# Kernel optimization log

Hardware: AMD Instinct MI355X
Metric: run time of the kernel (lower is better)

Reference implementation:

```python
import jax, jax.numpy as jnp
import numpy as np

N, D_IN, H, C, K = 16384, 2048, 4096, 256, 256


def setup_inputs() -> dict:
    key = jax.random.key(0)
    ks = jax.random.split(key, 13)

    def lin(kw, kb, fan_in, fan_out):
        # torch Linear default init: U(-1/sqrt(fan_in), 1/sqrt(fan_in)); stored as [in, out]
        bound = 1.0 / np.sqrt(fan_in)
        W = jax.random.uniform(kw, (fan_in, fan_out), jnp.float32, -bound, bound)
        b = jax.random.uniform(kb, (fan_out,), jnp.float32, -bound, bound)
        return W, b

    W_e1, b_e1 = lin(ks[0], ks[1], D_IN, H)
    W_e2, b_e2 = lin(ks[2], ks[3], H, C)
    W_d1, b_d1 = lin(ks[4], ks[5], C, H)
    W_d2, b_d2 = lin(ks[6], ks[7], H, D_IN)
    # codebooks init U(-1/K, 1/K) per the torch code
    cb1 = jax.random.uniform(ks[8], (K, C), jnp.float32, -1.0 / K, 1.0 / K)
    cb2 = jax.random.uniform(ks[9], (K, C), jnp.float32, -1.0 / K, 1.0 / K)
    cb3 = jax.random.uniform(ks[10], (K, C), jnp.float32, -1.0 / K, 1.0 / K)
    x = jax.random.normal(ks[11], (N, D_IN), jnp.float32)
    return {"x": x, "W_e1": W_e1, "b_e1": b_e1, "W_e2": W_e2, "b_e2": b_e2,
            "cb1": cb1, "cb2": cb2, "cb3": cb3,
            "W_d1": W_d1, "b_d1": b_d1, "W_d2": W_d2, "b_d2": b_d2}


def _vq_stage(z, cb):
    # dist[n,k] = sum_c (cb[k,c] - z[n,c])^2 = ||z||^2 - 2 z.cb^T + ||cb||^2
    # (same math as the torch N x K x C broadcast, expressed as a GEMM)
    d = (jnp.sum(z * z, axis=1, keepdims=True)
         - 2.0 * (z @ cb.T)
         + jnp.sum(cb * cb, axis=1))            # [N, K]
    nearest = jnp.argmin(d, axis=1)             # [N]
    zq = cb[nearest]                            # gather [N, C]
    return nearest, zq


def reference(x, W_e1, b_e1, W_e2, b_e2, cb1, cb2, cb3, W_d1, b_d1, W_d2, b_d2):
    ze_1 = jax.nn.relu(x @ W_e1 + b_e1) @ W_e2 + b_e2     # [N, C]
    nearest_1, zq_1 = _vq_stage(ze_1, cb1)
    ze_2 = ze_1 - zq_1
    nearest_2, zq_2 = _vq_stage(ze_2, cb2)
    ze_3 = ze_2 - zq_2
    nearest_3, zq_3 = _vq_stage(ze_3, cb3)
    # straight-through estimator
    decoder_input = ze_1 + jax.lax.stop_gradient(zq_1 + zq_2 + zq_3 - ze_1)
    x_hat = jax.nn.sigmoid(decoder_input @ W_d1 + b_d1) @ W_d2 + b_d2
    return (x_hat, ze_1, ze_2, ze_3, zq_1, zq_2, zq_3, nearest_1, nearest_2, nearest_3)
```

## Files before the change

kernel.cpp:

```cpp
#include <hip/hip_runtime.h>
#include <cstddef>


#define NN 16384
#define DIN 2048
#define HH 4096
#define CC 256
#define QRED ((size_t)4096 * 256)
#define NZ 24

typedef unsigned short ushortT;
typedef __attribute__((ext_vector_type(8))) short bf16x8;
typedef __attribute__((ext_vector_type(4))) float f32x4;

__device__ __forceinline__ ushortT f2b(float v) {
    unsigned int u = __float_as_uint(v);
    return (ushortT)((u + 0x7fffu + ((u >> 16) & 1u)) >> 16);
}
__device__ __forceinline__ float b2f(ushortT s) {
    return __uint_as_float(((unsigned int)s) << 16);
}
__device__ __forceinline__ void split3(float v, ushortT& h, ushortT& m, ushortT& l) {
    h = f2b(v);
    float r1 = v - b2f(h);
    m = f2b(r1);
    l = f2b(r1 - b2f(m));
}

__device__ __forceinline__ void gld16(const void* g, void* l) {
    __builtin_amdgcn_global_load_lds(
        (const __attribute__((address_space(1))) unsigned int*)g,
        (__attribute__((address_space(3))) unsigned int*)l,
        16, 0, 0);
}

template<int NP>
__launch_bounds__(256)
__global__ void tsplit(const float* __restrict__ W,
                       ushortT* __restrict__ T0,
                       ushortT* __restrict__ T1,
                       ushortT* __restrict__ T2,
                       int K, int N)
{
    __shared__ float tile[32][33];
    const int k0 = blockIdx.y * 32, n0 = blockIdx.x * 32;
    const int c = threadIdx.x & 31, r = threadIdx.x >> 5;
    #pragma unroll
    for (int i = 0; i < 4; ++i)
        tile[r + 8*i][c] = W[(size_t)(k0 + r + 8*i) * N + n0 + c];
    __syncthreads();
    #pragma unroll
    for (int i = 0; i < 4; ++i) {
        const int nl = r + 8*i, kl = c;
        float v = tile[kl][nl];
        size_t o = (size_t)(n0 + nl) * K + k0 + kl;
        ushortT h = f2b(v);
        T0[o] = h;
        if (NP > 1) {
            float r1 = v - b2f(h);
            ushortT m = f2b(r1);
            T1[o] = m;
            T2[o] = f2b(r1 - b2f(m));
        }
    }
}

__launch_bounds__(256)
__global__ void split_src(const float* __restrict__ X,
                          ushortT* __restrict__ P0, ushortT* __restrict__ P1,
                          ushortT* __restrict__ P2, size_t n4)
{
    for (size_t i = (size_t)blockIdx.x * 256 + threadIdx.x; i < n4;
         i += (size_t)gridDim.x * 256) {
        float4 v = *(const float4*)(X + i * 4);
        ushort4 hv, mv, lv;
        split3(v.x, ((ushortT*)&hv)[0], ((ushortT*)&mv)[0], ((ushortT*)&lv)[0]);
        split3(v.y, ((ushortT*)&hv)[1], ((ushortT*)&mv)[1], ((ushortT*)&lv)[1]);
        split3(v.z, ((ushortT*)&hv)[2], ((ushortT*)&mv)[2], ((ushortT*)&lv)[2]);
        split3(v.w, ((ushortT*)&hv)[3], ((ushortT*)&mv)[3], ((ushortT*)&lv)[3]);
        *(ushort4*)(P0 + i * 4) = hv;
        *(ushort4*)(P1 + i * 4) = mv;
        *(ushort4*)(P2 + i * 4) = lv;
    }
}

template<int NSEG, int KSH, int NTC, int EPI, int OM>
__launch_bounds__(512, 2)
__global__ void gemm256(const ushortT* __restrict__ Ab, size_t aPl,
                        const ushortT* __restrict__ Bb, size_t bPl,
                        const float* __restrict__ bias,
                        float* __restrict__ Cf,
                        ushortT* __restrict__ Ob, size_t oPl,
                        int N, int K)
{
    __shared__ ushortT sh[65536];

    const int t    = threadIdx.x;
    const int lane = t & 63;
    const int wid  = t >> 6;
    const int l15  = lane & 15;
    const int l4   = lane >> 4;
    const int bm   = blockIdx.y * 256;
    const int bn   = blockIdx.x * 256;
    const int wm   = (wid >> 2) * 128;
    const int wn   = (wid & 3) * 64;
    const int t0   = (OM == 3) ? blockIdx.z * NTC : 0;

    constexpr unsigned PA_PACK = 0x210100u;
    constexpr unsigned PB_PACK = 0x012010u;

    const int trow = t >> 3;
    const unsigned tcol = (unsigned)(((t & 7) ^ (trow & 7)) * 8);
    unsigned gA[4], gB[4];
    #pragma unroll
    for (int i = 0; i < 4; ++i) {
        gA[i] = (unsigned)(bm + i * 64 + trow) * (unsigned)K + tcol;
        gB[i] = (unsigned)(bn + i * 64 + trow) * (unsigned)K + tcol;
    }
    const int ldsT = t * 8;

    auto stageH = [&](int buf, int gtt, int half) {
        const int seg = (NSEG > 1) ? (gtt >> KSH) : 0;
        const unsigned kin = ((unsigned)(gtt & ((1 << KSH) - 1))) << 6;
        const unsigned pa = (NSEG > 1) ? ((PA_PACK >> (seg * 4)) & 15u) : 0u;
        const unsigned pb = (NSEG > 1) ? ((PB_PACK >> (seg * 4)) & 15u) : 0u;
        const ushortT* Abase = Ab + (size_t)pa * aPl + kin;
        const ushortT* Bbase = Bb + (size_t)pb * bPl + kin;
        ushortT* lb = sh + buf * 32768;
        if (half == 0) {
            gld16(Abase + gA[0], lb + 0 * 4096 + ldsT);
            gld16(Abase + gA[2], lb + 2 * 4096 + ldsT);
            gld16(Bbase + gB[0], lb + 16384 + 0 * 4096 + ldsT);
            gld16(Bbase + gB[1], lb + 16384 + 1 * 4096 + ldsT);
        } else {
            gld16(Bbase + gB[2], lb + 16384 + 2 * 4096 + ldsT);
            gld16(Bbase + gB[3], lb + 16384 + 3 * 4096 + ldsT);
            gld16(Abase + gA[1], lb + 1 * 4096 + ldsT);
            gld16(Abase + gA[3], lb + 3 * 4096 + ldsT);
        }
    };

    f32x4 acc[8][4] = {};

    stageH(0, t0, 0);
    stageH(0, t0, 1);

    #pragma unroll 1
    for (int tt = 0; tt < NTC; ++tt) {
        const int buf = tt & 1;
        const ushortT* As = sh + buf * 32768;
        const ushortT* Bs = As + 16384;
        const bool notlast = (tt + 1 < NTC);
        bf16x8 b0[4], a0[4], a1[4], b1[4], a2[4], a3[4];

        asm volatile("s_waitcnt vmcnt(0)" ::: "memory");
        __builtin_amdgcn_sched_barrier(0);
        __builtin_amdgcn_s_barrier();
        __builtin_amdgcn_sched_barrier(0);

        #pragma unroll
        for (int ni = 0; ni < 4; ++ni) {
            const int rb = wn + ni * 16 + l15;
            b0[ni] = *(const bf16x8*)&Bs[rb * 64 + (l4 ^ (rb & 7)) * 8];
        }
        #pragma unroll
        for (int mi = 0; mi < 4; ++mi) {
            const int ra = wm + mi * 16 + l15;
            a0[mi] = *(const bf16x8*)&As[ra * 64 + (l4 ^ (ra & 7)) * 8];
        }
        if (notlast) stageH(buf ^ 1, t0 + tt + 1, 0);
        __builtin_amdgcn_sched_barrier(0);
        __builtin_amdgcn_s_barrier();
        asm volatile("s_waitcnt lgkmcnt(0)" ::: "memory");
        __builtin_amdgcn_sched_barrier(0);
        __builtin_amdgcn_s_setprio(1);
        #pragma unroll
        for (int mi = 0; mi < 4; ++mi)
            #pragma unroll
            for (int ni = 0; ni < 4; ++ni)
                acc[mi][ni] = __builtin_amdgcn_mfma_f32_16x16x32_bf16(
                    a0[mi], b0[ni], acc[mi][ni], 0, 0, 0);
        __builtin_amdgcn_s_setprio(0);
        __builtin_amdgcn_sched_barrier(0);

        #pragma unroll
        for (int mi = 0; mi < 4; ++mi) {
            const int ra = wm + (mi + 4) * 16 + l15;
            a1[mi] = *(const bf16x8*)&As[ra * 64 + (l4 ^ (ra & 7)) * 8];
        }
        if (notlast) stageH(buf ^ 1, t0 + tt + 1, 1);
        __builtin_amdgcn_sched_barrier(0);
        __builtin_amdgcn_s_barrier();
        asm volatile("s_waitcnt lgkmcnt(0)" ::: "memory");
        __builtin_amdgcn_sched_barrier(0);
        __builtin_amdgcn_s_setprio(1);
        #pragma unroll
        for (int mi = 0; mi < 4; ++mi)
            #pragma unroll
            for (int ni = 0; ni < 4; ++ni)
                acc[mi + 4][ni] = __builtin_amdgcn_mfma_f32_16x16x32_bf16(
                    a1[mi], b0[ni], acc[mi + 4][ni], 0, 0, 0);
        __builtin_amdgcn_s_setprio(0);
        __builtin_amdgcn_sched_barrier(0);

        #pragma unroll
        for (int ni = 0; ni < 4; ++ni) {
            const int rb = wn + ni * 16 + l15;
            b1[ni] = *(const bf16x8*)&Bs[rb * 64 + ((4 | l4) ^ (rb & 7)) * 8];
        }
        #pragma unroll
        for (int mi = 0; mi < 4; ++mi) {
            const int ra = wm + mi * 16 + l15;
            a2[mi] = *(const bf16x8*)&As[ra * 64 + ((4 | l4) ^ (ra & 7)) * 8];
        }
        __builtin_amdgcn_sched_barrier(0);
        __builtin_amdgcn_s_barrier();
        asm volatile("s_waitcnt lgkmcnt(0)" ::: "memory");
        __builtin_amdgcn_sched_barrier(0);
        __builtin_amdgcn_s_setprio(1);
        #pragma unroll
        for (int mi = 0; mi < 4; ++mi)
            #pragma unroll
            for (int ni = 0; ni < 4; ++ni)
                acc[mi][ni] = __builtin_amdgcn_mfma_f32_16x16x32_bf16(
                    a2[mi], b1[ni], acc[mi][ni], 0, 0, 0);
        __builtin_amdgcn_s_setprio(0);
        __builtin_amdgcn_sched_barrier(0);

        #pragma unroll
        for (int mi = 0; mi < 4; ++mi) {
            const int ra = wm + (mi + 4) * 16 + l15;
            a3[mi] = *(const bf16x8*)&As[ra * 64 + ((4 | l4) ^ (ra & 7)) * 8];
        }
        __builtin_amdgcn_sched_barrier(0);
        __builtin_amdgcn_s_barrier();
        asm volatile("s_waitcnt lgkmcnt(0)" ::: "memory");
        __builtin_amdgcn_sched_barrier(0);
        __builtin_amdgcn_s_setprio(1);
        #pragma unroll
        for (int mi = 0; mi < 4; ++mi)
            #pragma unroll
            for (int ni = 0; ni < 4; ++ni)
                acc[mi + 4][ni] = __builtin_amdgcn_mfma_f32_16x16x32_bf16(
                    a3[mi], b1[ni], acc[mi + 4][ni], 0, 0, 0);
        __builtin_amdgcn_s_setprio(0);
        __builtin_amdgcn_sched_barrier(0);
    }

    #pragma unroll
    for (int ni = 0; ni < 4; ++ni) {
        const int gcol = bn + wn + ni * 16 + l15;
        float bvv = 0.0f;
        if (OM != 3) bvv = bias[gcol];
        #pragma unroll
        for (int mi = 0; mi < 8; ++mi) {
            #pragma unroll
            for (int r = 0; r < 4; ++r) {
                const int grow = bm + wm + mi * 16 + l4 * 4 + r;
                const size_t o = (size_t)grow * N + gcol;
                if (OM == 3) {
                    Cf[(size_t)blockIdx.z * oPl + o] = acc[mi][ni][r];
                } else {
                    float v = acc[mi][ni][r] + bvv;
                    if (EPI == 1) v = fmaxf(v, 0.0f);
                    if (EPI == 2) v = 1.0f / (1.0f + expf(-v));
                    if (OM == 0) {
                        Cf[o] = v;
                    } else if (OM == 2) {
                        Ob[o] = f2b(v);
                    } else {
                        ushortT hh, mm, ll;
                        split3(v, hh, mm, ll);
                        Ob[o] = hh; Ob[oPl + o] = mm; Ob[2 * oPl + o] = ll;
                    }
                }
            }
        }
    }
}

__launch_bounds__(256)
__global__ void reduce_z(const float* __restrict__ part,
                         const float* __restrict__ bias,
                         float* __restrict__ outp, int n4)
{
    const int i = blockIdx.x * 256 + threadIdx.x;
    if (i >= n4) return;
    float4 s = *(const float4*)(part + (size_t)i * 4);
    #pragma unroll
    for (int z = 1; z < NZ; ++z) {
        float4 p = *(const float4*)(part + (size_t)z * (QRED) + (size_t)i * 4);
        s.x = __fadd_rn(s.x, p.x); s.y = __fadd_rn(s.y, p.y);
        s.z = __fadd_rn(s.z, p.z); s.w = __fadd_rn(s.w, p.w);
    }
    const int c4 = (i * 4) & 255;
    float4 b = *(const float4*)(bias + c4);
    s.x = __fadd_rn(s.x, b.x); s.y = __fadd_rn(s.y, b.y);
    s.z = __fadd_rn(s.z, b.z); s.w = __fadd_rn(s.w, b.w);
    *(float4*)(outp + (size_t)i * 4) = s;
}

__launch_bounds__(256)
__global__ void vq_kernel(const float* __restrict__ ze1,
                          const float* __restrict__ cb1,
                          const float* __restrict__ cb2,
                          const float* __restrict__ cb3,
                          float* __restrict__ out_ze2, float* __restrict__ out_ze3,
                          float* __restrict__ out_zq1, float* __restrict__ out_zq2,
                          float* __restrict__ out_zq3,
                          float* __restrict__ out_n1,  float* __restrict__ out_n2,
                          float* __restrict__ out_n3,
                          ushortT* __restrict__ dec_p)
{
    __shared__ float Zs[16][260];
    __shared__ float Ds[16][260];
    __shared__ float DecS[16][260];
    __shared__ float Srow[16];
    __shared__ int   Kmin[16];

    const int t    = threadIdx.x;
    const int row0 = blockIdx.x * 16;

    for (int i = t; i < 16*64; i += 256) {
        int r = i >> 6, c4 = (i & 63) << 2;
        float4 v = *(const float4*)(ze1 + (size_t)(row0 + r) * 256 + c4);
        *(float4*)&Zs[r][c4] = v;
        float4 z = {0.f,0.f,0.f,0.f};
        *(float4*)&DecS[r][c4] = z;
    }
    __syncthreads();

    const float* cbs[3] = {cb1, cb2, cb3};
    float* zqs[3] = {out_zq1, out_zq2, out_zq3};
    float* nss[3] = {out_n1, out_n2, out_n3};

    for (int s = 0; s < 3; ++s) {
        const float* cb = cbs[s];
        if (t < 16) {
            float ssum = 0.f;
            for (int c = 0; c < 256; ++c) ssum = fmaf(Zs[t][c], Zs[t][c], ssum);
            Srow[t] = ssum;
        }
        __syncthreads();
        {
            float accr[16];
            #pragma unroll
            for (int r = 0; r < 16; ++r) accr[r] = 0.f;
            float c2 = 0.f;
            const float* cbrow = cb + (size_t)t * 256;
            for (int c4 = 0; c4 < 256; c4 += 4) {
                float4 cv = *(const float4*)(cbrow + c4);
                c2 = fmaf(cv.x,cv.x,fmaf(cv.y,cv.y,fmaf(cv.z,cv.z,fmaf(cv.w,cv.w,c2))));
                #pragma unroll
                for (int r = 0; r < 16; ++r) {
                    float4 zv = *(const float4*)&Zs[r][c4];
                    accr[r] = fmaf(zv.x,cv.x,fmaf(zv.y,cv.y,
                              fmaf(zv.z,cv.z,fmaf(zv.w,cv.w,accr[r]))));
                }
            }
            #pragma unroll
            for (int r = 0; r < 16; ++r) {
                float g2 = __fmul_rn(2.0f, accr[r]);
                float t1 = __fsub_rn(Srow[r], g2);
                Ds[r][t]  = __fadd_rn(t1, c2);
            }
        }
        __syncthreads();
        if (t < 16) {
            float best = Ds[t][0];
            int bk = 0;
            for (int k = 1; k < 256; ++k) {
                float v = Ds[t][k];
                if (v < best) { best = v; bk = k; }
            }
            Kmin[t] = bk;
            nss[s][row0 + t] = (float)bk;
        }
        __syncthreads();
        for (int i = t; i < 16*64; i += 256) {
            int r = i >> 6, c4 = (i & 63) << 2;
            const float* q = cb + (size_t)Kmin[r] * 256 + c4;
            float4 qv = *(const float4*)q;
            *(float4*)&zqs[s][(size_t)(row0 + r) * 256 + c4] = qv;
            float4 dv = *(float4*)&DecS[r][c4];
            dv.x = __fadd_rn(dv.x, qv.x); dv.y = __fadd_rn(dv.y, qv.y);
            dv.z = __fadd_rn(dv.z, qv.z); dv.w = __fadd_rn(dv.w, qv.w);
            *(float4*)&DecS[r][c4] = dv;
            if (s < 2) {
                float4 zv = *(float4*)&Zs[r][c4];
                zv.x = __fsub_rn(zv.x, qv.x); zv.y = __fsub_rn(zv.y, qv.y);
                zv.z = __fsub_rn(zv.z, qv.z); zv.w = __fsub_rn(zv.w, qv.w);
                *(float4*)&Zs[r][c4] = zv;
                float* oz = (s == 0) ? out_ze2 : out_ze3;
                *(float4*)&oz[(size_t)(row0 + r) * 256 + c4] = zv;
            }
        }
        __syncthreads();
    }

    for (int i = t; i < 16*64; i += 256) {
        int r = i >> 6, c4 = (i & 63) << 2;
        float4 z1 = *(const float4*)(ze1 + (size_t)(row0 + r) * 256 + c4);
        float4 dv = *(float4*)&DecS[r][c4];
        float4 o;
        o.x = __fadd_rn(z1.x, __fsub_rn(dv.x, z1.x));
        o.y = __fadd_rn(z1.y, __fsub_rn(dv.y, z1.y));
        o.z = __fadd_rn(z1.z, __fsub_rn(dv.z, z1.z));
        o.w = __fadd_rn(z1.w, __fsub_rn(dv.w, z1.w));
        ushort4 ov;
        ((ushortT*)&ov)[0] = f2b(o.x);
        ((ushortT*)&ov)[1] = f2b(o.y);
        ((ushortT*)&ov)[2] = f2b(o.z);
        ((ushortT*)&ov)[3] = f2b(o.w);
        *(ushort4*)(dec_p + (size_t)(row0 + r) * 256 + c4) = ov;
    }
}

extern "C" void kernel_launch(void* const* d_in, const int* in_sizes, int n_in,
                              void* d_out, int out_size, void* d_ws, size_t ws_size,
                              hipStream_t stream)
{
    const float* x   = (const float*)d_in[0];
    const float* We1 = (const float*)d_in[1];
    const float* be1 = (const float*)d_in[2];
    const float* We2 = (const float*)d_in[3];
    const float* be2 = (const float*)d_in[4];
    const float* cb1 = (const float*)d_in[5];
    const float* cb2 = (const float*)d_in[6];
    const float* cb3 = (const float*)d_in[7];
    const float* Wd1 = (const float*)d_in[8];
    const float* bd1 = (const float*)d_in[9];
    const float* Wd2 = (const float*)d_in[10];
    const float* bd2 = (const float*)d_in[11];

    float* out   = (float*)d_out;
    float* x_hat = out;
    float* ze1   = out + 33554432;
    float* ze2   = out + 37748736;
    float* ze3   = out + 41943040;
    float* zq1   = out + 46137344;
    float* zq2   = out + 50331648;
    float* zq3   = out + 54525952;
    float* n1    = out + 58720256;
    float* n2    = out + 58736640;
    float* n3    = out + 58753024;

    const int    QR   = 4096;
    const size_t szXq = (size_t)QR * DIN;
    const size_t szHq = (size_t)QR * HH;
    const size_t szW1 = (size_t)HH * DIN;
    const size_t szW2 = (size_t)CC * HH;

    ushortT* xq   = (ushortT*)d_ws;
    ushortT* hq   = xq + 3 * szXq;
    ushortT* We1t = hq + 3 * szHq;
    ushortT* We2t = We1t + 3 * szW1;
    ushortT* Wd1t = We2t + 3 * szW2;
    ushortT* Wd2t = Wd1t + szW2;
    ushortT* decp = Wd2t + szW1;
    float*   zpart = (float*)(decp + (size_t)NN * CC);
    ushortT* h2p  = xq;

    dim3 blk(256), blk5(512);

    tsplit<3><<<dim3(HH/32, DIN/32), blk, 0, stream>>>(We1, We1t, We1t+szW1, We1t+2*szW1, DIN, HH);
    tsplit<3><<<dim3(CC/32, HH/32),  blk, 0, stream>>>(We2, We2t, We2t+szW2, We2t+2*szW2, HH, CC);
    tsplit<1><<<dim3(HH/32, CC/32),  blk, 0, stream>>>(Wd1, Wd1t, nullptr, nullptr, CC, HH);
    tsplit<1><<<dim3(DIN/32, HH/32), blk, 0, stream>>>(Wd2, Wd2t, nullptr, nullptr, HH, DIN);

    for (int q = 0; q < 4; ++q) {
        split_src<<<dim3(2048), blk, 0, stream>>>(x + (size_t)q * szXq,
                                                  xq, xq + szXq, xq + 2*szXq, szXq / 4);
        gemm256<6,5,192,1,1><<<dim3(HH/256, QR/256), blk5, 0, stream>>>(
            xq, szXq, We1t, szW1, be1, nullptr, hq, szHq, HH, DIN);
        gemm256<6,6,16,0,3><<<dim3(CC/256, QR/256, NZ), blk5, 0, stream>>>(
            hq, szHq, We2t, szW2, nullptr, zpart, nullptr, QRED, CC, HH);
        reduce_z<<<dim3(QR*CC/4/256), blk, 0, stream>>>(
            zpart, be2, ze1 + (size_t)q * QR * CC, QR*CC/4);
    }

    vq_kernel<<<dim3(NN/16), blk, 0, stream>>>(ze1, cb1, cb2, cb3,
                                               ze2, ze3, zq1, zq2, zq3,
                                               n1, n2, n3, decp);

    gemm256<1,2,4,2,2><<<dim3(HH/256, NN/256), blk5, 0, stream>>>(
        decp, 0, Wd1t, 0, bd1, nullptr, h2p, 0, HH, CC);
    gemm256<1,6,64,0,0><<<dim3(DIN/256, NN/256), blk5, 0, stream>>>(
        h2p, 0, Wd2t, 0, bd2, x_hat, nullptr, 0, DIN, HH);
}
```

Before: 2.435 ms.

## Split GEMM global loads into quarter stages with cross-iteration prefetch and retune split-K

The double-buffered GEMM main loop now issues global-to-LDS loads in four quarter stages. The first quarter of tile tt+2 is prefetched into the buffer being drained, and partial vmcnt waits replace the full vmcnt(0) drain at the top of each iteration. This is meant to keep more memory traffic in flight and hide load latency behind the MFMA phases. It adds extra workgroup barriers after each MFMA phase to protect buffer reuse. Separately, the split-K encoder GEMM goes from 24 to 16 z-slices with 24 k-tiles each, trading less parallelism for fewer partial sums to reduce.

```diff
diff --git a/kernel.cpp b/kernel.cpp
--- a/kernel.cpp
+++ b/kernel.cpp
@@ -7,7 +7,7 @@
 #define HH 4096
 #define CC 256
 #define QRED ((size_t)4096 * 256)
-#define NZ 24
+#define NZ 16
 
 typedef unsigned short ushortT;
 typedef __attribute__((ext_vector_type(8))) short bf16x8;
@@ -119,7 +119,7 @@
     }
     const int ldsT = t * 8;
 
-    auto stageH = [&](int buf, int gtt, int half) {
+    auto stageS = [&](int buf, int gtt, int s) {
         const int seg = (NSEG > 1) ? (gtt >> KSH) : 0;
         const unsigned kin = ((unsigned)(gtt & ((1 << KSH) - 1))) << 6;
         const unsigned pa = (NSEG > 1) ? ((PA_PACK >> (seg * 4)) & 15u) : 0u;
@@ -127,14 +127,16 @@
         const ushortT* Abase = Ab + (size_t)pa * aPl + kin;
         const ushortT* Bbase = Bb + (size_t)pb * bPl + kin;
         ushortT* lb = sh + buf * 32768;
-        if (half == 0) {
+        if (s == 0) {
+            gld16(Bbase + gB[0], lb + 16384 + 0 * 4096 + ldsT);
+            gld16(Bbase + gB[1], lb + 16384 + 1 * 4096 + ldsT);
+        } else if (s == 1) {
+            gld16(Bbase + gB[2], lb + 16384 + 2 * 4096 + ldsT);
+            gld16(Bbase + gB[3], lb + 16384 + 3 * 4096 + ldsT);
+        } else if (s == 2) {
             gld16(Abase + gA[0], lb + 0 * 4096 + ldsT);
             gld16(Abase + gA[2], lb + 2 * 4096 + ldsT);
-            gld16(Bbase + gB[0], lb + 16384 + 0 * 4096 + ldsT);
-            gld16(Bbase + gB[1], lb + 16384 + 1 * 4096 + ldsT);
         } else {
-            gld16(Bbase + gB[2], lb + 16384 + 2 * 4096 + ldsT);
-            gld16(Bbase + gB[3], lb + 16384 + 3 * 4096 + ldsT);
             gld16(Abase + gA[1], lb + 1 * 4096 + ldsT);
             gld16(Abase + gA[3], lb + 3 * 4096 + ldsT);
         }
@@ -142,21 +144,28 @@
 
     f32x4 acc[8][4] = {};
 
-    stageH(0, t0, 0);
-    stageH(0, t0, 1);
+    stageS(0, t0, 0);
+    stageS(0, t0, 1);
+    stageS(0, t0, 2);
+    stageS(0, t0, 3);
+    if (NTC > 1) {
+        stageS(1, t0 + 1, 0);
+        asm volatile("s_waitcnt vmcnt(4)" ::: "memory");
+    } else {
+        asm volatile("s_waitcnt vmcnt(2)" ::: "memory");
+    }
+    __builtin_amdgcn_sched_barrier(0);
+    __builtin_amdgcn_s_barrier();
+    __builtin_amdgcn_sched_barrier(0);
 
     #pragma unroll 1
     for (int tt = 0; tt < NTC; ++tt) {
         const int buf = tt & 1;
         const ushortT* As = sh + buf * 32768;
         const ushortT* Bs = As + 16384;
-        const bool notlast = (tt + 1 < NTC);
+        const bool h1 = (tt + 1 < NTC);
+        const bool h2 = (tt + 2 < NTC);
         bf16x8 b0[4], a0[4], a1[4], b1[4], a2[4], a3[4];
-
-        asm volatile("s_waitcnt vmcnt(0)" ::: "memory");
-        __builtin_amdgcn_sched_barrier(0);
-        __builtin_amdgcn_s_barrier();
-        __builtin_amdgcn_sched_barrier(0);
 
         #pragma unroll
         for (int ni = 0; ni < 4; ++ni) {
@@ -168,7 +177,9 @@
             const int ra = wm + mi * 16 + l15;
             a0[mi] = *(const bf16x8*)&As[ra * 64 + (l4 ^ (ra & 7)) * 8];
         }
-        if (notlast) stageH(buf ^ 1, t0 + tt + 1, 0);
+        if (h1) stageS(buf ^ 1, t0 + tt + 1, 1);
+        if (h1) { asm volatile("s_waitcnt vmcnt(4)" ::: "memory"); }
+        else    { asm volatile("s_waitcnt vmcnt(0)" ::: "memory"); }
         __builtin_amdgcn_sched_barrier(0);
         __builtin_amdgcn_s_barrier();
         asm volatile("s_waitcnt lgkmcnt(0)" ::: "memory");
@@ -182,13 +193,15 @@
                     a0[mi], b0[ni], acc[mi][ni], 0, 0, 0);
         __builtin_amdgcn_s_setprio(0);
         __builtin_amdgcn_sched_barrier(0);
+        __builtin_amdgcn_s_barrier();
+        __builtin_amdgcn_sched_barrier(0);
 
         #pragma unroll
         for (int mi = 0; mi < 4; ++mi) {
             const int ra = wm + (mi + 4) * 16 + l15;
             a1[mi] = *(const bf16x8*)&As[ra * 64 + (l4 ^ (ra & 7)) * 8];
         }
-        if (notlast) stageH(buf ^ 1, t0 + tt + 1, 1);
+        if (h1) stageS(buf ^ 1, t0 + tt + 1, 2);
         __builtin_amdgcn_sched_barrier(0);
         __builtin_amdgcn_s_barrier();
         asm volatile("s_waitcnt lgkmcnt(0)" ::: "memory");
@@ -202,6 +215,8 @@
                     a1[mi], b0[ni], acc[mi + 4][ni], 0, 0, 0);
         __builtin_amdgcn_s_setprio(0);
         __builtin_amdgcn_sched_barrier(0);
+        __builtin_amdgcn_s_barrier();
+        __builtin_amdgcn_sched_barrier(0);
 
         #pragma unroll
         for (int ni = 0; ni < 4; ++ni) {
@@ -213,6 +228,7 @@
             const int ra = wm + mi * 16 + l15;
             a2[mi] = *(const bf16x8*)&As[ra * 64 + ((4 | l4) ^ (ra & 7)) * 8];
         }
+        if (h1) stageS(buf ^ 1, t0 + tt + 1, 3);
         __builtin_amdgcn_sched_barrier(0);
         __builtin_amdgcn_s_barrier();
         asm volatile("s_waitcnt lgkmcnt(0)" ::: "memory");
@@ -226,12 +242,18 @@
                     a2[mi], b1[ni], acc[mi][ni], 0, 0, 0);
         __builtin_amdgcn_s_setprio(0);
         __builtin_amdgcn_sched_barrier(0);
+        __builtin_amdgcn_s_barrier();
+        __builtin_amdgcn_sched_barrier(0);
 
         #pragma unroll
         for (int mi = 0; mi < 4; ++mi) {
             const int ra = wm + (mi + 4) * 16 + l15;
             a3[mi] = *(const bf16x8*)&As[ra * 64 + ((4 | l4) ^ (ra & 7)) * 8];
         }
+        if (h2) stageS(buf, t0 + tt + 2, 0);
+        if (h2)      { asm volatile("s_waitcnt vmcnt(4)" ::: "memory"); }
+        else if (h1) { asm volatile("s_waitcnt vmcnt(2)" ::: "memory"); }
+        else         { asm volatile("s_waitcnt vmcnt(0)" ::: "memory"); }
         __builtin_amdgcn_sched_barrier(0);
         __builtin_amdgcn_s_barrier();
         asm volatile("s_waitcnt lgkmcnt(0)" ::: "memory");
@@ -244,6 +266,8 @@
                 acc[mi + 4][ni] = __builtin_amdgcn_mfma_f32_16x16x32_bf16(
                     a3[mi], b1[ni], acc[mi + 4][ni], 0, 0, 0);
         __builtin_amdgcn_s_setprio(0);
+        __builtin_amdgcn_sched_barrier(0);
+        __builtin_amdgcn_s_barrier();
         __builtin_amdgcn_sched_barrier(0);
     }
 
@@ -473,7 +497,7 @@
                                                   xq, xq + szXq, xq + 2*szXq, szXq / 4);
         gemm256<6,5,192,1,1><<<dim3(HH/256, QR/256), blk5, 0, stream>>>(
             xq, szXq, We1t, szW1, be1, nullptr, hq, szHq, HH, DIN);
-        gemm256<6,6,16,0,3><<<dim3(CC/256, QR/256, NZ), blk5, 0, stream>>>(
+        gemm256<6,6,24,0,3><<<dim3(CC/256, QR/256, NZ), blk5, 0, stream>>>(
             hq, szHq, We2t, szW2, nullptr, zpart, nullptr, QRED, CC, HH);
         reduce_z<<<dim3(QR*CC/4/256), blk, 0, stream>>>(
             zpart, be2, ze1 + (size_t)q * QR * CC, QR*CC/4);
```

New measurement: 2.453 ms. About the same (+0.7%).
